# Optimization experiments

Measured on AMD Instinct MI355X. Metric: run time of the kernel, lower is better.

Reference implementation:

```python
import jax, jax.numpy as jnp
import numpy as np

ALPHA = 1.0


def _bce_with_logits(x, y):
    # numerically stable mean BCEWithLogitsLoss
    return jnp.mean(jnp.maximum(x, 0.0) - x * y + jnp.log1p(jnp.exp(-jnp.abs(x))))


def setup_inputs() -> dict:
    key = jax.random.key(0)
    k1, k2, k3, k4, k5, k6 = jax.random.split(key, 6)
    B, T, S = 2097152, 5, 16
    return {
        "y_pred_binary": jax.random.normal(k1, (B,), dtype=jnp.float32),
        "y_pred_type": jax.random.normal(k2, (B, T), dtype=jnp.float32),
        "y_pred_source": jax.random.normal(k3, (B, S), dtype=jnp.float32),
        "y_true_binary": jax.random.randint(k4, (B,), 0, 2).astype(jnp.float32),
        "y_true_type": jax.random.randint(k5, (B, T), 0, 2).astype(jnp.float32),
        "y_true_source": jax.random.randint(k6, (B,), 0, S, dtype=jnp.int32),
    }


def reference(y_pred_binary, y_pred_type, y_pred_source,
              y_true_binary, y_true_type, y_true_source):
    # task A: binary BCE
    loss = _bce_with_logits(y_pred_binary, y_true_binary)
    # task B: type BCE (unbalanced branch = plain mean BCE over all elements)
    loss = loss + _bce_with_logits(y_pred_type, y_true_type)
    # task C: source cross-entropy (mean over batch)
    logp = jax.nn.log_softmax(y_pred_source, axis=1)  # [B, S]
    ce = -jnp.mean(jnp.take_along_axis(logp, y_true_source[:, None], axis=1))
    loss = loss + ce
    # consistency terms: round(sigmoid(x)) == (x > 0); count disagreements (vectorized XOR)
    b_cls = y_pred_binary > 0.0                      # [B]
    t_cls = y_pred_type[:, 0] > 0.0                  # [B]
    s_cls = jnp.argmax(y_pred_source, axis=1) > 0    # [B]
    loss = loss + ALPHA * jnp.mean((b_cls ^ t_cls).astype(jnp.float32))
    loss = loss + ALPHA * jnp.mean((b_cls ^ s_cls).astype(jnp.float32))
    return loss
```

## Files before the change

### kernel.cpp

```cpp
#include <hip/hip_runtime.h>
#include <math.h>


#define NBLOCKS 2048
#define NTHREADS 256

__device__ __forceinline__ float bce_term(float x, float y) {
    return fmaxf(x, 0.0f) - x * y + __logf(1.0f + __expf(-fabsf(x)));
}

__global__ __launch_bounds__(NTHREADS, 2) void mtl_partial_kernel(
    const float* __restrict__ pb,
    const float* __restrict__ pt,
    const float* __restrict__ ps,
    const float* __restrict__ tb,
    const float* __restrict__ tt,
    const int*   __restrict__ ts,
    double* __restrict__ partial,
    int B)
{
    const int tid = blockIdx.x * NTHREADS + threadIdx.x;
    const int stride = NBLOCKS * NTHREADS;

    float acc = 0.0f;

    for (int i = tid; i < B; i += stride) {
        const float xb = pb[i];
        const float yb = tb[i];
        const int   t  = ts[i];
        const float t0 = pt[(size_t)i * 5];

        float c = fmaxf(xb, 0.0f) - xb * yb + __logf(1.0f + __expf(-fabsf(xb)));

        float xs[16];
        const float4* ps4 = reinterpret_cast<const float4*>(ps + (size_t)i * 16);
        #pragma unroll
        for (int q = 0; q < 4; ++q) {
            const float4 v = ps4[q];
            xs[q * 4 + 0] = v.x;
            xs[q * 4 + 1] = v.y;
            xs[q * 4 + 2] = v.z;
            xs[q * 4 + 3] = v.w;
        }
        float m15 = xs[1];
        #pragma unroll
        for (int j = 2; j < 16; ++j) m15 = fmaxf(m15, xs[j]);
        const float m = fmaxf(xs[0], m15);

        float se = 0.0f;
        float xt = 0.0f;
        #pragma unroll
        for (int j = 0; j < 16; ++j) {
            se += __expf(xs[j] - m);
            xt = (j == t) ? xs[j] : xt;
        }
        c += m + __logf(se) - xt;

        const bool bc = xb > 0.0f;
        c += (bc != (t0 > 0.0f)) ? 1.0f : 0.0f;
        c += (bc != (m15 > xs[0])) ? 1.0f : 0.0f;

        acc += c;
    }

    {
        const int n  = B * 5;
        const int n4 = n >> 2;
        const float4* pt4 = reinterpret_cast<const float4*>(pt);
        const float4* tt4 = reinterpret_cast<const float4*>(tt);
        float accB = 0.0f;
        for (int i = tid; i < n4; i += stride) {
            const float4 x = pt4[i];
            const float4 y = tt4[i];
            accB += bce_term(x.x, y.x);
            accB += bce_term(x.y, y.y);
            accB += bce_term(x.z, y.z);
            accB += bce_term(x.w, y.w);
        }
        for (int i = (n4 << 2) + tid; i < n; i += stride)
            accB += bce_term(pt[i], tt[i]);
        acc += accB * 0.2f;
    }

    float a = acc;
    #pragma unroll
    for (int off = 32; off > 0; off >>= 1)
        a += __shfl_down(a, off, 64);

    __shared__ double smem[NTHREADS / 64];
    const int lane = threadIdx.x & 63;
    const int wave = threadIdx.x >> 6;
    if (lane == 0) smem[wave] = (double)a;
    __syncthreads();
    if (threadIdx.x == 0) {
        double s = 0.0;
        #pragma unroll
        for (int w = 0; w < NTHREADS / 64; ++w) s += smem[w];
        partial[blockIdx.x] = s;
    }
}

__global__ __launch_bounds__(NTHREADS) void mtl_final_kernel(
    const double* __restrict__ partial, float* __restrict__ out, int nblocks, int B)
{
    double acc = 0.0;
    for (int i = threadIdx.x; i < nblocks; i += NTHREADS)
        acc += partial[i];
    #pragma unroll
    for (int off = 32; off > 0; off >>= 1)
        acc += __shfl_down(acc, off, 64);
    __shared__ double smem[NTHREADS / 64];
    const int lane = threadIdx.x & 63;
    const int wave = threadIdx.x >> 6;
    if (lane == 0) smem[wave] = acc;
    __syncthreads();
    if (threadIdx.x == 0) {
        double s = 0.0;
        #pragma unroll
        for (int w = 0; w < NTHREADS / 64; ++w) s += smem[w];
        out[0] = (float)(s / (double)B);
    }
}

extern "C" void kernel_launch(void* const* d_in, const int* in_sizes, int n_in,
                              void* d_out, int out_size, void* d_ws, size_t ws_size,
                              hipStream_t stream) {
    const float* pb = (const float*)d_in[0];
    const float* pt = (const float*)d_in[1];
    const float* ps = (const float*)d_in[2];
    const float* tb = (const float*)d_in[3];
    const float* tt = (const float*)d_in[4];
    const int*   ts = (const int*)d_in[5];
    float* out = (float*)d_out;
    const int B = in_sizes[0];

    double* partial = (double*)d_ws;

    mtl_partial_kernel<<<NBLOCKS, NTHREADS, 0, stream>>>(pb, pt, ps, tb, tt, ts, partial, B);
    mtl_final_kernel<<<1, NTHREADS, 0, stream>>>(partial, out, NBLOCKS, B);
}
```

Baseline: 49.85 us.

## Stage source and type rows through swizzled LDS with register prefetch

Each block now loads contiguous tiles of the source logits and of the type predictions and targets with coalesced float4 loads, then transposes them through XOR-swizzled shared memory so each thread reads its own row. This replaces the strided per-row float4 loads and the separate pass over the type arrays, which re-read pt. The next tile is prefetched into registers while the current one is computed, and launch bounds rise to 4 blocks per SM. The fast path applies only when B equals exactly 4*NBLOCKS*NTHREADS, and it adds two barriers per iteration plus extra register pressure.

Result: slower. 151.8 us (+204.6%).

```diff
diff --git a/kernel.cpp b/kernel.cpp
--- a/kernel.cpp
+++ b/kernel.cpp
@@ -5,11 +5,38 @@
 #define NBLOCKS 2048
 #define NTHREADS 256
 
+#define PS_B 16384
+#define PT_B 5120
+#define LDS_BYTES (PS_B + 2 * PT_B)
+
 __device__ __forceinline__ float bce_term(float x, float y) {
     return fmaxf(x, 0.0f) - x * y + __logf(1.0f + __expf(-fabsf(x)));
 }
 
-__global__ __launch_bounds__(NTHREADS, 2) void mtl_partial_kernel(
+__device__ __forceinline__ float row_math(const float xs[16], float xb, float yb,
+                                          int tg, float pt0, float bsum) {
+    float m15 = xs[1];
+    #pragma unroll
+    for (int j = 2; j < 16; ++j) m15 = fmaxf(m15, xs[j]);
+    const float m = fmaxf(xs[0], m15);
+
+    float se = 0.0f;
+    float xt = 0.0f;
+    #pragma unroll
+    for (int j = 0; j < 16; ++j) {
+        se += __expf(xs[j] - m);
+        xt = (j == tg) ? xs[j] : xt;
+    }
+    float c = fmaxf(xb, 0.0f) - xb * yb + __logf(1.0f + __expf(-fabsf(xb)));
+    c += m + __logf(se) - xt;
+    c += bsum * 0.2f;
+    const bool bc = xb > 0.0f;
+    c += (bc != (pt0 > 0.0f)) ? 1.0f : 0.0f;
+    c += (bc != (m15 > xs[0])) ? 1.0f : 0.0f;
+    return c;
+}
+
+__global__ __launch_bounds__(NTHREADS, 4) void mtl_partial_kernel(
     const float* __restrict__ pb,
     const float* __restrict__ pt,
     const float* __restrict__ ps,
@@ -19,80 +46,129 @@
     double* __restrict__ partial,
     int B)
 {
-    const int tid = blockIdx.x * NTHREADS + threadIdx.x;
-    const int stride = NBLOCKS * NTHREADS;
-
+    __shared__ __align__(16) unsigned char lds[LDS_BYTES];
+    __shared__ double smem[NTHREADS / 64];
+
+    const int t = threadIdx.x;
     float acc = 0.0f;
 
-    for (int i = tid; i < B; i += stride) {
-        const float xb = pb[i];
-        const float yb = tb[i];
-        const int   t  = ts[i];
-        const float t0 = pt[(size_t)i * 5];
-
-        float c = fmaxf(xb, 0.0f) - xb * yb + __logf(1.0f + __expf(-fabsf(xb)));
-
-        float xs[16];
-        const float4* ps4 = reinterpret_cast<const float4*>(ps + (size_t)i * 16);
-        #pragma unroll
-        for (int q = 0; q < 4; ++q) {
-            const float4 v = ps4[q];
-            xs[q * 4 + 0] = v.x;
-            xs[q * 4 + 1] = v.y;
-            xs[q * 4 + 2] = v.z;
-            xs[q * 4 + 3] = v.w;
+    if (B == 4 * NBLOCKS * NTHREADS) {
+        const float4* psf4 = reinterpret_cast<const float4*>(ps);
+        const float4* ptf4 = reinterpret_cast<const float4*>(pt);
+        const float4* ttf4 = reinterpret_cast<const float4*>(tt);
+
+        float4 ps_r[4], pt_r[2], tt_r[2];
+
+        {
+            const size_t R0 = (size_t)blockIdx.x * NTHREADS;
+            const size_t psb = R0 * 4;
+            const size_t ptb = (R0 / 4) * 5;
+            #pragma unroll
+            for (int q = 0; q < 4; ++q) ps_r[q] = psf4[psb + t + 256 * q];
+            pt_r[0] = ptf4[ptb + t];
+            tt_r[0] = ttf4[ptb + t];
+            if (t < 64) {
+                pt_r[1] = ptf4[ptb + 256 + t];
+                tt_r[1] = ttf4[ptb + 256 + t];
+            }
         }
-        float m15 = xs[1];
-        #pragma unroll
-        for (int j = 2; j < 16; ++j) m15 = fmaxf(m15, xs[j]);
-        const float m = fmaxf(xs[0], m15);
-
-        float se = 0.0f;
-        float xt = 0.0f;
-        #pragma unroll
-        for (int j = 0; j < 16; ++j) {
-            se += __expf(xs[j] - m);
-            xt = (j == t) ? xs[j] : xt;
+
+        for (int k = 0; k < 4; ++k) {
+            const size_t R0 = (size_t)k * NBLOCKS * NTHREADS
+                            + (size_t)blockIdx.x * NTHREADS;
+
+            __syncthreads();
+            #pragma unroll
+            for (int q = 0; q < 4; ++q) {
+                const int g   = t + 256 * q;
+                const int off = (g * 16) ^ (((g >> 2) & 7) << 4);
+                *reinterpret_cast<float4*>(lds + off) = ps_r[q];
+            }
+            *reinterpret_cast<float4*>(lds + PS_B + t * 16)        = pt_r[0];
+            *reinterpret_cast<float4*>(lds + PS_B + PT_B + t * 16) = tt_r[0];
+            if (t < 64) {
+                *reinterpret_cast<float4*>(lds + PS_B + (256 + t) * 16)        = pt_r[1];
+                *reinterpret_cast<float4*>(lds + PS_B + PT_B + (256 + t) * 16) = tt_r[1];
+            }
+            __syncthreads();
+
+            if (k < 3) {
+                const size_t R1 = R0 + (size_t)NBLOCKS * NTHREADS;
+                const size_t psb = R1 * 4;
+                const size_t ptb = (R1 / 4) * 5;
+                #pragma unroll
+                for (int q = 0; q < 4; ++q) ps_r[q] = psf4[psb + t + 256 * q];
+                pt_r[0] = ptf4[ptb + t];
+                tt_r[0] = ttf4[ptb + t];
+                if (t < 64) {
+                    pt_r[1] = ptf4[ptb + 256 + t];
+                    tt_r[1] = ttf4[ptb + 256 + t];
+                }
+            }
+
+            const size_t r = R0 + t;
+            const float xb = pb[r];
+            const float yb = tb[r];
+            const int   tg = ts[r];
+
+            float xs[16];
+            #pragma unroll
+            for (int q = 0; q < 4; ++q) {
+                const int off = (t * 64 + q * 16) ^ ((t & 7) << 4);
+                const float4 v = *reinterpret_cast<const float4*>(lds + off);
+                xs[q * 4 + 0] = v.x;
+                xs[q * 4 + 1] = v.y;
+                xs[q * 4 + 2] = v.z;
+                xs[q * 4 + 3] = v.w;
+            }
+            const float* ldsf = reinterpret_cast<const float*>(lds);
+            float bsum = 0.0f;
+            float pt0  = 0.0f;
+            #pragma unroll
+            for (int j = 0; j < 5; ++j) {
+                const float x = ldsf[(PS_B >> 2) + t * 5 + j];
+                const float y = ldsf[((PS_B + PT_B) >> 2) + t * 5 + j];
+                if (j == 0) pt0 = x;
+                bsum += bce_term(x, y);
+            }
+            acc += row_math(xs, xb, yb, tg, pt0, bsum);
         }
-        c += m + __logf(se) - xt;
-
-        const bool bc = xb > 0.0f;
-        c += (bc != (t0 > 0.0f)) ? 1.0f : 0.0f;
-        c += (bc != (m15 > xs[0])) ? 1.0f : 0.0f;
-
-        acc += c;
-    }
-
-    {
-        const int n  = B * 5;
-        const int n4 = n >> 2;
-        const float4* pt4 = reinterpret_cast<const float4*>(pt);
-        const float4* tt4 = reinterpret_cast<const float4*>(tt);
-        float accB = 0.0f;
-        for (int i = tid; i < n4; i += stride) {
-            const float4 x = pt4[i];
-            const float4 y = tt4[i];
-            accB += bce_term(x.x, y.x);
-            accB += bce_term(x.y, y.y);
-            accB += bce_term(x.z, y.z);
-            accB += bce_term(x.w, y.w);
+    } else {
+        const int stride = NBLOCKS * NTHREADS;
+        for (int i = blockIdx.x * NTHREADS + t; i < B; i += stride) {
+            const float xb = pb[i];
+            const float yb = tb[i];
+            const int   tg = ts[i];
+            float xs[16];
+            const float4* ps4 = reinterpret_cast<const float4*>(ps + (size_t)i * 16);
+            #pragma unroll
+            for (int q = 0; q < 4; ++q) {
+                const float4 v = ps4[q];
+                xs[q * 4 + 0] = v.x; xs[q * 4 + 1] = v.y;
+                xs[q * 4 + 2] = v.z; xs[q * 4 + 3] = v.w;
+            }
+            float bsum = 0.0f, pt0 = 0.0f;
+            #pragma unroll
+            for (int j = 0; j < 5; ++j) {
+                const float x = pt[(size_t)i * 5 + j];
+                const float y = tt[(size_t)i * 5 + j];
+                if (j == 0) pt0 = x;
+                bsum += bce_term(x, y);
+            }
+            acc += row_math(xs, xb, yb, tg, pt0, bsum);
         }
-        for (int i = (n4 << 2) + tid; i < n; i += stride)
-            accB += bce_term(pt[i], tt[i]);
-        acc += accB * 0.2f;
+        __syncthreads();
     }
 
     float a = acc;
     #pragma unroll
     for (int off = 32; off > 0; off >>= 1)
         a += __shfl_down(a, off, 64);
-
-    __shared__ double smem[NTHREADS / 64];
-    const int lane = threadIdx.x & 63;
-    const int wave = threadIdx.x >> 6;
+    const int lane = t & 63;
+    const int wave = t >> 6;
     if (lane == 0) smem[wave] = (double)a;
     __syncthreads();
-    if (threadIdx.x == 0) {
+    if (t == 0) {
         double s = 0.0;
         #pragma unroll
         for (int w = 0; w < NTHREADS / 64; ++w) s += smem[w];
```
